# Optimization experiments

Measured on AMD Instinct MI355X. Metric: run time of the kernel, lower is better.

The kernel has to match this reference:

```python
import jax, jax.numpy as jnp
import numpy as np

N_NODES = 6144
N_EDGES = 196608
IN_F = 256
OUT_F = 128
EDGE_D = 16
ALPHA = 0.2  # LeakyReLU negative slope
NEG_INF = -1e12


def setup_inputs() -> dict:
    key = jax.random.key(0)
    k0, k1, k2, k3, k4 = jax.random.split(key, 5)
    input_h = jax.random.normal(k0, (N_NODES, IN_F), dtype=jnp.float32)
    edge_index = jax.random.randint(k1, (2, N_EDGES), 0, N_NODES, dtype=jnp.int64)
    edge_features = jax.random.normal(k2, (N_EDGES, EDGE_D), dtype=jnp.float32)
    W = jax.random.normal(k3, (IN_F, OUT_F), dtype=jnp.float32) * 0.1
    a = jax.random.normal(k4, (2 * OUT_F + EDGE_D, 1), dtype=jnp.float32) * 0.1
    return {"input_h": input_h, "edge_index": edge_index,
            "edge_features": edge_features, "W": W, "a": a}


def reference(input_h, edge_index, edge_features, W, a):
    # h = X W : [N, OUT_F]
    h = input_h @ W
    N, F = h.shape
    # split attention vector: concat([h_i, h_j, e_ij]) @ a == h_i@a1 + h_j@a2 + e_ij@a3
    a1 = a[:F, 0]
    a2 = a[F:2 * F, 0]
    a3 = a[2 * F:, 0]
    src, dst = edge_index[0], edge_index[1]
    # dense adjacency mask and per-edge-feature score scattered into N x N
    adj = jnp.zeros((N, N), dtype=bool).at[src, dst].set(True)
    edge_score = jnp.zeros((N, N), dtype=h.dtype).at[src, dst].set(edge_features @ a3)
    # e[i, j] = leaky_relu(h_i @ a1 + h_j @ a2 + edge_score[i, j])
    e = jax.nn.leaky_relu((h @ a1)[:, None] + (h @ a2)[None, :] + edge_score,
                          negative_slope=ALPHA)
    attention = jax.nn.softmax(jnp.where(adj, e, NEG_INF), axis=1)
    # dropout is identity in eval mode (p applied only when training)
    return attention @ h
```

## Files before the change

### kernel.cpp

```cpp
#include <hip/hip_runtime.h>
#include <hip/hip_bf16.h>

#define N_NODES 6144
#define N_EDGES 196608
#define IN_F    256
#define OUT_F   128
#define EDGE_D  16
#define ALPHA   0.2f
#define ROW_CAP 128

#define F_X  0
#define F_EF 1
#define F_W  2
#define F_A  3
#define F_EI 4

typedef __hip_bfloat16 bf16;
typedef __attribute__((ext_vector_type(8))) short short8;
typedef __attribute__((ext_vector_type(4))) short short4v;
typedef __attribute__((ext_vector_type(4))) float f32x4;
typedef __attribute__((ext_vector_type(2))) float f32x2;

__device__ __forceinline__ float loadf(const void* __restrict__ p, int idx, int isf32) {
    return isf32 ? ((const float*)p)[idx]
                 : __bfloat162float(((const bf16*)p)[idx]);
}
__device__ __forceinline__ unsigned short f2bf_bits(float f) {
    union { bf16 h; unsigned short u; } cv;
    cv.h = __float2bfloat16(f);
    return cv.u;
}
__device__ __forceinline__ int get_src(const int* __restrict__ ei, int k, int l64) {
    return l64 ? ei[2 * k] : ei[k];
}
__device__ __forceinline__ int get_dst(const int* __restrict__ ei, int k, int l64) {
    return l64 ? ei[2 * N_EDGES + 2 * k] : ei[N_EDGES + k];
}
__device__ __forceinline__ int probe_f32(const unsigned* __restrict__ w, int lane) {
    unsigned u = w[lane];
    int e = (u >> 7) & 0xff;
    unsigned long long b = __ballot(e >= 99 && e <= 155);
    return (__popcll(b) >= 48) ? 0 : 1;
}

__global__ __launch_bounds__(256) void setup_kernel(const int* __restrict__ ei,
                                                    const void* __restrict__ X,
                                                    const void* __restrict__ ef,
                                                    const void* __restrict__ W,
                                                    const void* __restrict__ a,
                                                    int* __restrict__ cnt,
                                                    int* __restrict__ flags,
                                                    bf16* __restrict__ Wt) {
    const int b = blockIdx.x, t = threadIdx.x;
    const int lane = t & 63, wv = t >> 6;
    if (b < 24) {
        cnt[b * 256 + t] = 0;
        return;
    }
    if (b == 24) {
        if (wv == 0) {
            int v = ei[2 * lane + 1];
            unsigned long long bl = __ballot(v != 0);
            if (lane == 0) flags[F_EI] = (bl == 0ull) ? 1 : 0;
        } else if (wv == 1) {
            int r = probe_f32((const unsigned*)X, lane);
            if (lane == 0) flags[F_X] = r;
        } else if (wv == 2) {
            int r = probe_f32((const unsigned*)ef, lane);
            if (lane == 0) flags[F_EF] = r;
        } else {
            int r = probe_f32((const unsigned*)a, lane);
            if (lane == 0) flags[F_A] = r;
        }
        return;
    }
    int fw = probe_f32((const unsigned*)W, lane);
    int o = ((b - 25) * 256 + t) * 4;
#pragma unroll
    for (int j = 0; j < 4; ++j) {
        int oo = o + j;
        int n = oo >> 8, k = oo & 255;
        Wt[oo] = __float2bfloat16(loadf(W, k * OUT_F + n, fw));
    }
}

__global__ __launch_bounds__(256) void gemm_scatter_kernel(
        const void* __restrict__ X, const bf16* __restrict__ Wt,
        const void* __restrict__ a, const int* __restrict__ ei,
        const int* __restrict__ flags, float* __restrict__ H,
        float* __restrict__ s1, float* __restrict__ s2,
        int* __restrict__ cnt, int* __restrict__ edge_list) {
    __shared__ float red[2][4][16];
    const int bid = blockIdx.x, t = threadIdx.x;
    const int lane = t & 63, wv = t >> 6;

    if (bid >= 384) {
        const int l64 = flags[F_EI];
        if (!l64) {
            const int4* s4 = (const int4*)ei;
            for (int kb = (bid - 384) * 1024 + 4 * t; kb < N_EDGES; kb += 128 * 1024) {
                int4 s = s4[kb >> 2];
#pragma unroll
                for (int j = 0; j < 4; ++j) {
                    int src = (j == 0) ? s.x : (j == 1) ? s.y : (j == 2) ? s.z : s.w;
                    int pos = atomicAdd(&cnt[src], 1);
                    if (pos < ROW_CAP) edge_list[src * ROW_CAP + pos] = kb + j;
                }
            }
        } else {
            for (int kb = (bid - 384) * 1024 + 4 * t; kb < N_EDGES; kb += 128 * 1024) {
                int4 s0 = *(const int4*)(ei + 2 * kb);
                int4 s1v = *(const int4*)(ei + 2 * kb + 4);
#pragma unroll
                for (int j = 0; j < 4; ++j) {
                    int src = (j == 0) ? s0.x : (j == 1) ? s0.z : (j == 2) ? s1v.x : s1v.z;
                    int pos = atomicAdd(&cnt[src], 1);
                    if (pos < ROW_CAP) edge_list[src * ROW_CAP + pos] = kb + j;
                }
            }
        }
        return;
    }

    const int fx = flags[F_X], fa = flags[F_A];
    const int m0   = bid * 16;
    const int mrow = lane & 15;
    const int q    = lane >> 4;
    const int cb   = wv * 32;

    f32x4 acc0 = (f32x4){0.f, 0.f, 0.f, 0.f};
    f32x4 acc1 = (f32x4){0.f, 0.f, 0.f, 0.f};

    const bf16*  ap  = (const bf16*)X  + (m0 + mrow) * IN_F + q * 8;
    const float* apf = (const float*)X + (m0 + mrow) * IN_F + q * 8;
    const bf16*  bp  = Wt + (cb + mrow) * IN_F + q * 8;

#pragma unroll
    for (int ks = 0; ks < 8; ++ks) {
        const int k0 = ks * 32;
        short8 afr;
        if (!fx) {
            afr = *(const short8*)(ap + k0);
        } else {
            f32x4 u0 = *(const f32x4*)(apf + k0);
            f32x4 u1 = *(const f32x4*)(apf + k0 + 4);
#pragma unroll
            for (int j = 0; j < 4; ++j) {
                afr[j]     = (short)f2bf_bits(u0[j]);
                afr[4 + j] = (short)f2bf_bits(u1[j]);
            }
        }
        short8 b0 = *(const short8*)(bp + k0);
        short8 b1 = *(const short8*)(bp + 16 * IN_F + k0);
        acc0 = __builtin_amdgcn_mfma_f32_16x16x32_bf16(afr, b0, acc0, 0, 0, 0);
        acc1 = __builtin_amdgcn_mfma_f32_16x16x32_bf16(afr, b1, acc1, 0, 0, 0);
    }

    float p1[4] = {0.f, 0.f, 0.f, 0.f};
    float p2[4] = {0.f, 0.f, 0.f, 0.f};
#pragma unroll
    for (int g = 0; g < 2; ++g) {
        f32x4 acc = g ? acc1 : acc0;
        int col = cb + g * 16 + mrow;
        float a1v = loadf(a, col, fa);
        float a2v = loadf(a, OUT_F + col, fa);
#pragma unroll
        for (int r = 0; r < 4; ++r) {
            H[(m0 + q * 4 + r) * OUT_F + col] = acc[r];
            p1[r] += acc[r] * a1v;
            p2[r] += acc[r] * a2v;
        }
    }
#pragma unroll
    for (int off = 1; off < 16; off <<= 1)
#pragma unroll
        for (int r = 0; r < 4; ++r) {
            p1[r] += __shfl_xor(p1[r], off, 64);
            p2[r] += __shfl_xor(p2[r], off, 64);
        }
    if (mrow == 0)
#pragma unroll
        for (int r = 0; r < 4; ++r) {
            red[0][wv][q * 4 + r] = p1[r];
            red[1][wv][q * 4 + r] = p2[r];
        }
    __syncthreads();
    if (t < 16) {
        s1[m0 + t] = red[0][0][t] + red[0][1][t] + red[0][2][t] + red[0][3][t];
        s2[m0 + t] = red[1][0][t] + red[1][1][t] + red[1][2][t] + red[1][3][t];
    }
}

__global__ __launch_bounds__(256) void aggregate_kernel(const float* __restrict__ H,
                                                        const int* __restrict__ ei,
                                                        const void* __restrict__ ef,
                                                        const void* __restrict__ a,
                                                        const float* __restrict__ s1,
                                                        const float* __restrict__ s2,
                                                        const int* __restrict__ cnt,
                                                        const int* __restrict__ edge_list,
                                                        const int* __restrict__ flags,
                                                        void* __restrict__ out) {
    __shared__ int   s_pk[4][ROW_CAP];
    __shared__ float s_lg[4][ROW_CAP];
    const int lane = threadIdx.x & 63;
    const int w    = threadIdx.x >> 6;
    const int row  = blockIdx.x * 4 + w;
    const int l64  = flags[F_EI];
    const int fe   = flags[F_EF];
    const int fa   = flags[F_A];
    const int fo   = flags[F_X];
    const int n    = min(cnt[row], ROW_CAP);
    const int base = row * ROW_CAP;
    const int half = lane >> 5;
    const int c4   = (lane & 31) * 4;

    float a3r[EDGE_D];
#pragma unroll
    for (int i = 0; i < EDGE_D; ++i) a3r[i] = loadf(a, 2 * OUT_F + i, fa);

    float denom = 0.f;
    f32x4 acc = (f32x4){0.f, 0.f, 0.f, 0.f};

    if (n == 0) {
        denom = 1.f;
    } else {
        const float s1row = s1[row];
        for (int i = lane; i < n; i += 64) {
            int k = edge_list[base + i];
            int d = get_dst(ei, k, l64);
            s_pk[w][i] = (d << 18) | k;
            float es = 0.f;
            if (!fe) {
                short8 v0 = *(const short8*)((const bf16*)ef + k * EDGE_D);
                short8 v1 = *(const short8*)((const bf16*)ef + k * EDGE_D + 8);
#pragma unroll
                for (int j = 0; j < 8; ++j) {
                    union { short s; bf16 h; } u0, u1;
                    u0.s = v0[j]; u1.s = v1[j];
                    es += __bfloat162float(u0.h) * a3r[j];
                    es += __bfloat162float(u1.h) * a3r[8 + j];
                }
            } else {
                const float* efp = (const float*)ef + k * EDGE_D;
#pragma unroll
                for (int j = 0; j < EDGE_D; ++j) es += efp[j] * a3r[j];
            }
            float x = s1row + s2[d] + es;
            s_lg[w][i] = x > 0.f ? x : ALPHA * x;
        }
        float wsum = 0.f;
        for (int i = lane; i < n; i += 64) {
            int pk = s_pk[w][i], d = pk >> 18;
            bool loser = false;
            for (int j = 0; j < n; ++j) {
                int pj = s_pk[w][j];
                if ((pj >> 18) == d && pj > pk) loser = true;
            }
            float wgt = loser ? 0.f : __expf(s_lg[w][i]);
            s_lg[w][i] = wgt;
            wsum += wgt;
        }
#pragma unroll
        for (int off = 32; off; off >>= 1) wsum += __shfl_xor(wsum, off, 64);
        denom = wsum;

        int i = 0;
        for (; i + 8 <= n; i += 8) {
            int ia = i + half,     ib = i + 2 + half;
            int ic = i + 4 + half, id = i + 6 + half;
            float wa = s_lg[w][ia], wb = s_lg[w][ib];
            float wc = s_lg[w][ic], wd = s_lg[w][id];
            int da = s_pk[w][ia] >> 18, db = s_pk[w][ib] >> 18;
            int dc = s_pk[w][ic] >> 18, dd = s_pk[w][id] >> 18;
            f32x4 ha = *(const f32x4*)(H + da * OUT_F + c4);
            f32x4 hb = *(const f32x4*)(H + db * OUT_F + c4);
            f32x4 hc = *(const f32x4*)(H + dc * OUT_F + c4);
            f32x4 hd = *(const f32x4*)(H + dd * OUT_F + c4);
#pragma unroll
            for (int j = 0; j < 4; ++j)
                acc[j] += wa * ha[j] + wb * hb[j] + wc * hc[j] + wd * hd[j];
        }
        for (; i + 2 <= n; i += 2) {
            int ia = i + half;
            float wa = s_lg[w][ia];
            int da = s_pk[w][ia] >> 18;
            f32x4 ha = *(const f32x4*)(H + da * OUT_F + c4);
#pragma unroll
            for (int j = 0; j < 4; ++j) acc[j] += wa * ha[j];
        }
        if (i < n && half == 0) {
            float wa = s_lg[w][i];
            int da = s_pk[w][i] >> 18;
            f32x4 ha = *(const f32x4*)(H + da * OUT_F + c4);
#pragma unroll
            for (int j = 0; j < 4; ++j) acc[j] += wa * ha[j];
        }
    }
#pragma unroll
    for (int j = 0; j < 4; ++j) acc[j] += __shfl_xor(acc[j], 32, 64);

    float inv = 1.f / denom;
    if (half == 0) {
        if (fo) {
            f32x4 r;
#pragma unroll
            for (int j = 0; j < 4; ++j) r[j] = acc[j] * inv;
            *(f32x4*)((float*)out + row * OUT_F + c4) = r;
        } else {
            short4v r;
#pragma unroll
            for (int j = 0; j < 4; ++j) r[j] = (short)f2bf_bits(acc[j] * inv);
            *(short4v*)((bf16*)out + row * OUT_F + c4) = r;
        }
    }
}

extern "C" void kernel_launch(void* const* d_in, const int* in_sizes, int n_in,
                              void* d_out, int out_size, void* d_ws, size_t ws_size,
                              hipStream_t stream) {
    const void* X  = d_in[0];
    const int*  ei = (const int*)d_in[1];
    const void* ef = d_in[2];
    const void* W  = d_in[3];
    const void* a  = d_in[4];
    void* out = d_out;

    char* p = (char*)d_ws;
    auto alloc = [&](size_t bytes) -> void* {
        void* r = (void*)p;
        p += (bytes + 255) & ~(size_t)255;
        return r;
    };
    int*   flags     = (int*)  alloc(256);
    float* H         = (float*)alloc((size_t)N_NODES * OUT_F * 4);
    float* s1        = (float*)alloc((size_t)N_NODES * 4);
    float* s2        = (float*)alloc((size_t)N_NODES * 4);
    int*   cnt       = (int*)  alloc((size_t)N_NODES * 4);
    int*   edge_list = (int*)  alloc((size_t)N_NODES * ROW_CAP * 4);
    bf16*  Wt        = (bf16*) alloc((size_t)OUT_F * IN_F * 2);

    size_t needed = (size_t)((char*)p - (char*)d_ws);
    if (ws_size < needed) return;

    setup_kernel<<<57, 256, 0, stream>>>(ei, X, ef, W, a, cnt, flags, Wt);
    gemm_scatter_kernel<<<512, 256, 0, stream>>>(X, Wt, a, ei, flags, H, s1, s2,
                                                 cnt, edge_list);
    aggregate_kernel<<<N_NODES / 4, 256, 0, stream>>>(H, ei, ef, a, s1, s2, cnt,
                                                      edge_list, flags, out);
}
```

Measured before the change: 100.8 us.

## Precompute edge scores and destinations during scatter, store packed in edge list

```diff
diff --git a/kernel.cpp b/kernel.cpp
--- a/kernel.cpp
+++ b/kernel.cpp
@@ -29,12 +29,6 @@
     union { bf16 h; unsigned short u; } cv;
     cv.h = __float2bfloat16(f);
     return cv.u;
-}
-__device__ __forceinline__ int get_src(const int* __restrict__ ei, int k, int l64) {
-    return l64 ? ei[2 * k] : ei[k];
-}
-__device__ __forceinline__ int get_dst(const int* __restrict__ ei, int k, int l64) {
-    return l64 ? ei[2 * N_EDGES + 2 * k] : ei[N_EDGES + k];
 }
 __device__ __forceinline__ int probe_f32(const unsigned* __restrict__ w, int lane) {
     unsigned u = w[lane];
@@ -87,36 +81,63 @@
 __global__ __launch_bounds__(256) void gemm_scatter_kernel(
         const void* __restrict__ X, const bf16* __restrict__ Wt,
         const void* __restrict__ a, const int* __restrict__ ei,
-        const int* __restrict__ flags, float* __restrict__ H,
-        float* __restrict__ s1, float* __restrict__ s2,
-        int* __restrict__ cnt, int* __restrict__ edge_list) {
+        const void* __restrict__ ef, const int* __restrict__ flags,
+        float* __restrict__ H, float* __restrict__ s1, float* __restrict__ s2,
+        int* __restrict__ cnt, int2* __restrict__ el2) {
     __shared__ float red[2][4][16];
     const int bid = blockIdx.x, t = threadIdx.x;
     const int lane = t & 63, wv = t >> 6;
 
     if (bid >= 384) {
         const int l64 = flags[F_EI];
-        if (!l64) {
-            const int4* s4 = (const int4*)ei;
-            for (int kb = (bid - 384) * 1024 + 4 * t; kb < N_EDGES; kb += 128 * 1024) {
-                int4 s = s4[kb >> 2];
-#pragma unroll
-                for (int j = 0; j < 4; ++j) {
-                    int src = (j == 0) ? s.x : (j == 1) ? s.y : (j == 2) ? s.z : s.w;
-                    int pos = atomicAdd(&cnt[src], 1);
-                    if (pos < ROW_CAP) edge_list[src * ROW_CAP + pos] = kb + j;
+        const int fe  = flags[F_EF];
+        const int fa  = flags[F_A];
+        float a3r[EDGE_D];
+#pragma unroll
+        for (int i = 0; i < EDGE_D; ++i) a3r[i] = loadf(a, 2 * OUT_F + i, fa);
+
+        for (int kb = (bid - 384) * 1024 + 4 * t; kb < N_EDGES; kb += 128 * 1024) {
+            int srcv[4], dstv[4];
+            if (!l64) {
+                int4 s = *(const int4*)(ei + kb);
+                int4 d = *(const int4*)(ei + N_EDGES + kb);
+                srcv[0] = s.x; srcv[1] = s.y; srcv[2] = s.z; srcv[3] = s.w;
+                dstv[0] = d.x; dstv[1] = d.y; dstv[2] = d.z; dstv[3] = d.w;
+            } else {
+                int4 s0 = *(const int4*)(ei + 2 * kb);
+                int4 s1q = *(const int4*)(ei + 2 * kb + 4);
+                int4 d0 = *(const int4*)(ei + 2 * N_EDGES + 2 * kb);
+                int4 d1 = *(const int4*)(ei + 2 * N_EDGES + 2 * kb + 4);
+                srcv[0] = s0.x; srcv[1] = s0.z; srcv[2] = s1q.x; srcv[3] = s1q.z;
+                dstv[0] = d0.x; dstv[1] = d0.z; dstv[2] = d1.x; dstv[3] = d1.z;
+            }
+            float e3v[4];
+#pragma unroll
+            for (int j = 0; j < 4; ++j) {
+                float es = 0.f;
+                if (!fe) {
+                    short8 v0 = *(const short8*)((const bf16*)ef + (kb + j) * EDGE_D);
+                    short8 v1 = *(const short8*)((const bf16*)ef + (kb + j) * EDGE_D + 8);
+#pragma unroll
+                    for (int jj = 0; jj < 8; ++jj) {
+                        union { short s; bf16 h; } u0, u1;
+                        u0.s = v0[jj]; u1.s = v1[jj];
+                        es += __bfloat162float(u0.h) * a3r[jj];
+                        es += __bfloat162float(u1.h) * a3r[8 + jj];
+                    }
+                } else {
+                    const float* efp = (const float*)ef + (kb + j) * EDGE_D;
+#pragma unroll
+                    for (int jj = 0; jj < EDGE_D; ++jj) es += efp[jj] * a3r[jj];
                 }
-            }
-        } else {
-            for (int kb = (bid - 384) * 1024 + 4 * t; kb < N_EDGES; kb += 128 * 1024) {
-                int4 s0 = *(const int4*)(ei + 2 * kb);
-                int4 s1v = *(const int4*)(ei + 2 * kb + 4);
-#pragma unroll
-                for (int j = 0; j < 4; ++j) {
-                    int src = (j == 0) ? s0.x : (j == 1) ? s0.z : (j == 2) ? s1v.x : s1v.z;
-                    int pos = atomicAdd(&cnt[src], 1);
-                    if (pos < ROW_CAP) edge_list[src * ROW_CAP + pos] = kb + j;
-                }
+                e3v[j] = es;
+            }
+#pragma unroll
+            for (int j = 0; j < 4; ++j) {
+                int pos = atomicAdd(&cnt[srcv[j]], 1);
+                if (pos < ROW_CAP)
+                    el2[srcv[j] * ROW_CAP + pos] =
+                        make_int2((dstv[j] << 18) | (kb + j), __float_as_int(e3v[j]));
             }
         }
         return;
@@ -192,13 +213,10 @@
 }
 
 __global__ __launch_bounds__(256) void aggregate_kernel(const float* __restrict__ H,
-                                                        const int* __restrict__ ei,
-                                                        const void* __restrict__ ef,
-                                                        const void* __restrict__ a,
                                                         const float* __restrict__ s1,
                                                         const float* __restrict__ s2,
                                                         const int* __restrict__ cnt,
-                                                        const int* __restrict__ edge_list,
+                                                        const int2* __restrict__ el2,
                                                         const int* __restrict__ flags,
                                                         void* __restrict__ out) {
     __shared__ int   s_pk[4][ROW_CAP];
@@ -206,19 +224,12 @@
     const int lane = threadIdx.x & 63;
     const int w    = threadIdx.x >> 6;
     const int row  = blockIdx.x * 4 + w;
-    const int l64  = flags[F_EI];
-    const int fe   = flags[F_EF];
-    const int fa   = flags[F_A];
     const int fo   = flags[F_X];
     const int n    = min(cnt[row], ROW_CAP);
     const int base = row * ROW_CAP;
     const int half = lane >> 5;
     const int c4   = (lane & 31) * 4;
 
-    float a3r[EDGE_D];
-#pragma unroll
-    for (int i = 0; i < EDGE_D; ++i) a3r[i] = loadf(a, 2 * OUT_F + i, fa);
-
     float denom = 0.f;
     f32x4 acc = (f32x4){0.f, 0.f, 0.f, 0.f};
 
@@ -227,26 +238,10 @@
     } else {
         const float s1row = s1[row];
         for (int i = lane; i < n; i += 64) {
-            int k = edge_list[base + i];
-            int d = get_dst(ei, k, l64);
-            s_pk[w][i] = (d << 18) | k;
-            float es = 0.f;
-            if (!fe) {
-                short8 v0 = *(const short8*)((const bf16*)ef + k * EDGE_D);
-                short8 v1 = *(const short8*)((const bf16*)ef + k * EDGE_D + 8);
-#pragma unroll
-                for (int j = 0; j < 8; ++j) {
-                    union { short s; bf16 h; } u0, u1;
-                    u0.s = v0[j]; u1.s = v1[j];
-                    es += __bfloat162float(u0.h) * a3r[j];
-                    es += __bfloat162float(u1.h) * a3r[8 + j];
-                }
-            } else {
-                const float* efp = (const float*)ef + k * EDGE_D;
-#pragma unroll
-                for (int j = 0; j < EDGE_D; ++j) es += efp[j] * a3r[j];
-            }
-            float x = s1row + s2[d] + es;
+            int2 el = el2[base + i];
+            int pk = el.x;
+            float x = s1row + s2[pk >> 18] + __int_as_float(el.y);
+            s_pk[w][i] = pk;
             s_lg[w][i] = x > 0.f ? x : ALPHA * x;
         }
         float wsum = 0.f;
@@ -337,15 +332,14 @@
     float* s1        = (float*)alloc((size_t)N_NODES * 4);
     float* s2        = (float*)alloc((size_t)N_NODES * 4);
     int*   cnt       = (int*)  alloc((size_t)N_NODES * 4);
-    int*   edge_list = (int*)  alloc((size_t)N_NODES * ROW_CAP * 4);
+    int2*  el2       = (int2*) alloc((size_t)N_NODES * ROW_CAP * 8);
     bf16*  Wt        = (bf16*) alloc((size_t)OUT_F * IN_F * 2);
 
     size_t needed = (size_t)((char*)p - (char*)d_ws);
     if (ws_size < needed) return;
 
     setup_kernel<<<57, 256, 0, stream>>>(ei, X, ef, W, a, cnt, flags, Wt);
-    gemm_scatter_kernel<<<512, 256, 0, stream>>>(X, Wt, a, ei, flags, H, s1, s2,
-                                                 cnt, edge_list);
-    aggregate_kernel<<<N_NODES / 4, 256, 0, stream>>>(H, ei, ef, a, s1, s2, cnt,
-                                                      edge_list, flags, out);
-}
+    gemm_scatter_kernel<<<512, 256, 0, stream>>>(X, Wt, a, ei, ef, flags, H, s1, s2,
+                                                 cnt, el2);
+    aggregate_kernel<<<N_NODES / 4, 256, 0, stream>>>(H, s1, s2, cnt, el2, flags, out);
+}
```

After: 103.7 us. 1.03x slower.
